# Kernel optimization log

Measured on AMD Instinct MI355X. Metric: run time of the kernel, lower is better.

Reference implementation:

```python
import jax, jax.numpy as jnp
import numpy as np

N_NODES = 100000
N_EDGES = 1600000
D_IN = 256
D_OUT = 128


def setup_inputs() -> dict:
    key = jax.random.key(0)
    ks = jax.random.split(key, 7)
    h = jax.random.normal(ks[0], (N_NODES, D_IN), dtype=jnp.float32)
    src = jax.random.randint(ks[1], (N_EDGES,), 0, N_NODES, dtype=jnp.int32)
    dst = jax.random.randint(ks[2], (N_EDGES,), 0, N_NODES, dtype=jnp.int32)
    W = jax.random.normal(ks[3], (D_IN, D_OUT), dtype=jnp.float32) * (1.0 / np.sqrt(D_IN))
    b = jax.random.normal(ks[4], (D_OUT,), dtype=jnp.float32) * 0.01
    w_att = jax.random.normal(ks[5], (2 * D_OUT, 1), dtype=jnp.float32) * (1.0 / np.sqrt(2 * D_OUT))
    b_att = jax.random.normal(ks[6], (1,), dtype=jnp.float32) * 0.01
    return {"h": h, "src": src, "dst": dst, "W": W, "b": b, "w_att": w_att, "b_att": b_att}


def reference(h, src, dst, W, b, w_att, b_att):
    # node projection: graph.ndata['h'] = self.linear(h)
    hp = h @ W + b  # [N, D_OUT]
    n = hp.shape[0]
    d = hp.shape[1]
    # edge attention: leaky_relu(att_linear(cat[h_src, h_dst]))
    # cat([hs, hd]) @ w_att == hs @ w_att[:d] + hd @ w_att[d:]  (avoids [E, 2d] concat)
    wa_s = w_att[:d, 0]  # [D_OUT]
    wa_d = w_att[d:, 0]  # [D_OUT]
    e = hp[src] @ wa_s + hp[dst] @ wa_d + b_att[0]  # [E]
    e = jax.nn.leaky_relu(e)  # default negative_slope 0.01 matches F.leaky_relu
    # segment softmax over each destination node's incoming edges
    emax = jax.ops.segment_max(e, dst, num_segments=n)  # [N]
    ex = jnp.exp(e - emax[dst])  # [E]
    denom = jax.ops.segment_sum(ex, dst, num_segments=n)  # [N]
    # weighted scatter-sum of src features: sum_e alpha_e * h_src_e
    num = jax.ops.segment_sum(ex[:, None] * hp[src], dst, num_segments=n)  # [N, D_OUT]
    out = num / jnp.where(denom > 0, denom, 1.0)[:, None]  # zero-in-degree nodes -> 0
    return out
```

## Files before the change

kernel.cpp:

```cpp
#include <hip/hip_runtime.h>
#include <hip/hip_bf16.h>

#define D_IN 256
#define D_OUT 128
#define BM 128
#define BNODES 64
#define BCAP 1536
#define EPB 8192
#define MAXNB 1600

typedef __attribute__((ext_vector_type(8))) short bf16x8;
typedef __attribute__((ext_vector_type(4))) float f32x4;

__device__ __forceinline__ unsigned short f2bf(float f) {
    unsigned u = __float_as_uint(f);
    unsigned r = ((u >> 16) & 1u) + 0x7FFFu;
    return (unsigned short)((u + r) >> 16);
}
__device__ __forceinline__ unsigned pk2(float a, float b) {
    return (unsigned)f2bf(a) | ((unsigned)f2bf(b) << 16);
}

__global__ __launch_bounds__(256) void init_bcursor_kernel(int* __restrict__ bcursor, int nb)
{
    int i = blockIdx.x * 256 + threadIdx.x;
    if (i < nb) bcursor[i] = i * BCAP;
}

__global__ __launch_bounds__(256) void prep_kernel(
    const float* __restrict__ W, unsigned short* __restrict__ WbT)
{
    int idx = blockIdx.x * 256 + threadIdx.x;
    int k = idx >> 7;
    int c = idx & 127;
    WbT[(size_t)c * 256 + k] = f2bf(W[idx]);
}

__global__ __launch_bounds__(256) void gemm_mfma_kernel(
    const float* __restrict__ h, const unsigned short* __restrict__ WbT,
    const float* __restrict__ b, const float* __restrict__ w_att,
    unsigned short* __restrict__ hpb,
    float* __restrict__ alpha_s, float* __restrict__ alpha_d, int n)
{
    __shared__ char lds[32768];
    __shared__ float als[2][BM], ald[2][BM];
    char* aT = lds;
    char* bT = lds + 16384;

    const int t    = threadIdx.x;
    const int row0 = blockIdx.x * BM;
    const int wv = t >> 6, lane = t & 63;
    const int wr = wv >> 1, wc = wv & 1;
    const int fr = lane & 15, fq = lane >> 4;

    f32x4 acc[4][4];
    #pragma unroll
    for (int m = 0; m < 4; ++m)
        #pragma unroll
        for (int nn = 0; nn < 4; ++nn) acc[m][nn] = (f32x4){0.f, 0.f, 0.f, 0.f};

    const int sr = t >> 1;
    const int sk = (t & 1) * 32;
    const size_t arow = (size_t)((row0 + sr < n) ? (row0 + sr) : (n - 1));
    const float*          asrc = h   + arow * D_IN + sk;
    const unsigned short* bsrc = WbT + (size_t)sr * D_IN + sk;
    const int   wbase = sr * 128 + sk * 2;
    const int   swz   = (sr & 7) << 4;

    for (int kb = 0; kb < 4; ++kb) {
        const float4* as = (const float4*)(asrc + kb * 64);
        #pragma unroll
        for (int c = 0; c < 4; ++c) {
            float4 v0 = as[2 * c], v1 = as[2 * c + 1];
            uint4 p;
            p.x = pk2(v0.x, v0.y); p.y = pk2(v0.z, v0.w);
            p.z = pk2(v1.x, v1.y); p.w = pk2(v1.z, v1.w);
            *(uint4*)(aT + ((wbase + c * 16) ^ swz)) = p;
        }
        const uint4* bs = (const uint4*)(bsrc + kb * 64);
        #pragma unroll
        for (int c = 0; c < 4; ++c)
            *(uint4*)(bT + ((wbase + c * 16) ^ swz)) = bs[c];
        __syncthreads();

        #pragma unroll
        for (int ks = 0; ks < 2; ++ks) {
            bf16x8 af[4], bfr[4];
            #pragma unroll
            for (int m = 0; m < 4; ++m) {
                int row = wr * 64 + m * 16 + fr;
                int o = row * 128 + ks * 64 + fq * 16;
                af[m] = *(const bf16x8*)(aT + (o ^ ((row & 7) << 4)));
            }
            #pragma unroll
            for (int nn = 0; nn < 4; ++nn) {
                int col = wc * 64 + nn * 16 + fr;
                int o = col * 128 + ks * 64 + fq * 16;
                bfr[nn] = *(const bf16x8*)(bT + (o ^ ((col & 7) << 4)));
            }
            #pragma unroll
            for (int m = 0; m < 4; ++m)
                #pragma unroll
                for (int nn = 0; nn < 4; ++nn)
                    acc[m][nn] = __builtin_amdgcn_mfma_f32_16x16x32_bf16(
                        af[m], bfr[nn], acc[m][nn], 0, 0, 0);
        }
        __syncthreads();
    }

    float bcol[4], was[4], wad[4];
    #pragma unroll
    for (int nn = 0; nn < 4; ++nn) {
        int j = wc * 64 + nn * 16 + fr;
        bcol[nn] = b[j];
        was[nn]  = w_att[j];
        wad[nn]  = w_att[D_OUT + j];
    }
    #pragma unroll
    for (int m = 0; m < 4; ++m) {
        #pragma unroll
        for (int reg = 0; reg < 4; ++reg) {
            const int lrow = wr * 64 + m * 16 + fq * 4 + reg;
            const int grow = row0 + lrow;
            float ps = 0.f, pd = 0.f;
            #pragma unroll
            for (int nn = 0; nn < 4; ++nn) {
                float vv = acc[m][nn][reg] + bcol[nn];
                ps += vv * was[nn];
                pd += vv * wad[nn];
                if (grow < n)
                    hpb[(size_t)grow * D_OUT + wc * 64 + nn * 16 + fr] = f2bf(vv);
            }
            #pragma unroll
            for (int o = 1; o < 16; o <<= 1) {
                ps += __shfl_xor(ps, o);
                pd += __shfl_xor(pd, o);
            }
            if (fr == 0) { als[wc][lrow] = ps; ald[wc][lrow] = pd; }
        }
    }
    __syncthreads();
    if (t < BM) {
        int grow = row0 + t;
        if (grow < n) {
            alpha_s[grow] = als[0][t] + als[1][t];
            alpha_d[grow] = ald[0][t] + ald[1][t];
        }
    }
}

__global__ __launch_bounds__(1024) void bucket_scatter_kernel(
    const int* __restrict__ src, const int* __restrict__ dst,
    const float* __restrict__ alpha_s, const float* __restrict__ alpha_d,
    const float* __restrict__ b_att, int* __restrict__ bcursor,
    int2* __restrict__ ebuf, int ne, int nb)
{
    __shared__ int lhist[MAXNB];
    __shared__ int gbase[MAXNB];
    __shared__ int lcur[MAXNB];
    const int t = threadIdx.x;
    for (int i = t; i < nb; i += 1024) { lhist[i] = 0; lcur[i] = 0; }
    __syncthreads();
    const int base = blockIdx.x * EPB;
    #pragma unroll
    for (int j = 0; j < EPB / 1024; ++j) {
        int idx = base + j * 1024 + t;
        if (idx < ne) atomicAdd(&lhist[dst[idx] >> 6], 1);
    }
    __syncthreads();
    for (int i = t; i < nb; i += 1024) {
        int c = lhist[i];
        gbase[i] = c ? atomicAdd(&bcursor[i], c) : 0;
    }
    __syncthreads();
    const float ba = b_att[0];
    #pragma unroll
    for (int j = 0; j < EPB / 1024; ++j) {
        int idx = base + j * 1024 + t;
        if (idx < ne) {
            int s = src[idx], d = dst[idx];
            float ev = alpha_s[s] + alpha_d[d] + ba;
            ev = (ev >= 0.f) ? ev : 0.01f * ev;
            int bkt = d >> 6;
            int pos = gbase[bkt] + atomicAdd(&lcur[bkt], 1);
            if (pos < (bkt + 1) * BCAP)
                ebuf[pos] = make_int2(s | ((d & 63) << 17), __float_as_int(ev));
        }
    }
}

#define ACCUM8(uvar, wvar)                                     \
    acc[0] += (wvar) * __uint_as_float((uvar).x << 16);        \
    acc[1] += (wvar) * __uint_as_float((uvar).x & 0xFFFF0000u);\
    acc[2] += (wvar) * __uint_as_float((uvar).y << 16);        \
    acc[3] += (wvar) * __uint_as_float((uvar).y & 0xFFFF0000u);\
    acc[4] += (wvar) * __uint_as_float((uvar).z << 16);        \
    acc[5] += (wvar) * __uint_as_float((uvar).z & 0xFFFF0000u);\
    acc[6] += (wvar) * __uint_as_float((uvar).w << 16);        \
    acc[7] += (wvar) * __uint_as_float((uvar).w & 0xFFFF0000u);

__global__ __launch_bounds__(512) void aggregate_kernel(
    const unsigned short* __restrict__ hpb, const int2* __restrict__ ebuf,
    const int* __restrict__ bcursor, float* __restrict__ out, int n)
{
    __shared__ int2 srec[BCAP];
    __shared__ int lhist[BNODES], lstart[BNODES], lcur[BNODES];
    const int t = threadIdx.x;
    const int bk = blockIdx.x;
    const int node0 = bk << 6;
    const int base = bk * BCAP;
    int cnt = bcursor[bk] - base;
    cnt = min(cnt, BCAP);

    if (t < BNODES) lhist[t] = 0;
    __syncthreads();
    for (int i = t; i < cnt; i += 512)
        atomicAdd(&lhist[(ebuf[base + i].x >> 17) & 63], 1);
    __syncthreads();
    if (t < BNODES) {
        int c0 = lhist[t];
        int incl = c0;
        #pragma unroll
        for (int o = 1; o < 64; o <<= 1) {
            int v = __shfl_up(incl, o);
            if (t >= o) incl += v;
        }
        lstart[t] = incl - c0;
        lcur[t]   = incl - c0;
    }
    __syncthreads();
    for (int i = t; i < cnt; i += 512) {
        int2 r = ebuf[base + i];
        int pos = atomicAdd(&lcur[(r.x >> 17) & 63], 1);
        srec[pos] = r;
    }
    __syncthreads();

    const int wv = t >> 6, lane = t & 63;
    const int q = lane >> 4, dlane = lane & 15;
    const uint4* hp4 = (const uint4*)hpb;

    #pragma unroll
    for (int k = 0; k < 8; ++k) {
        const int nd = wv * 8 + k;
        const int gnode = node0 + nd;
        const int off = lstart[nd], c = lhist[nd];
        float acc[8] = {0.f,0.f,0.f,0.f,0.f,0.f,0.f,0.f};
        float denom = 0.f;

        if (c > 0 && c <= 64) {
            int2 r = srec[off + min(lane, c - 1)];
            float ev = (lane < c) ? __int_as_float(r.y) : -INFINITY;
            int   sv = r.x & 0x1FFFF;
            float m = ev;
            #pragma unroll
            for (int o = 32; o; o >>= 1) m = fmaxf(m, __shfl_xor(m, o));
            float w = __expf(ev - m);
            denom = w;
            #pragma unroll
            for (int o = 32; o; o >>= 1) denom += __shfl_xor(denom, o);
            #pragma unroll 2
            for (int t0 = 0; t0 < c; t0 += 4) {
                int tt = t0 + q;
                float wq = __shfl(w, tt);
                int   sq = __shfl(sv, tt);
                uint4 u = hp4[(size_t)sq * 16 + dlane];
                ACCUM8(u, wq)
            }
            #pragma unroll
            for (int k2 = 0; k2 < 8; ++k2) {
                acc[k2] += __shfl_xor(acc[k2], 16);
                acc[k2] += __shfl_xor(acc[k2], 32);
            }
        } else if (c > 64) {
            float m = -INFINITY;
            for (int i = lane; i < c; i += 64)
                m = fmaxf(m, __int_as_float(srec[off + i].y));
            #pragma unroll
            for (int o = 32; o; o >>= 1) m = fmaxf(m, __shfl_xor(m, o));
            for (int t0 = 0; t0 < c; t0 += 4) {
                int tt = t0 + q;
                float wq = 0.f; int sq = 0;
                if (tt < c) {
                    int2 r = srec[off + tt];
                    sq = r.x & 0x1FFFF;
                    wq = __expf(__int_as_float(r.y) - m);
                }
                uint4 u = hp4[(size_t)sq * 16 + dlane];
                ACCUM8(u, wq)
                denom += wq;
            }
            #pragma unroll
            for (int k2 = 0; k2 < 8; ++k2) {
                acc[k2] += __shfl_xor(acc[k2], 16);
                acc[k2] += __shfl_xor(acc[k2], 32);
            }
            denom += __shfl_xor(denom, 16);
            denom += __shfl_xor(denom, 32);
        }

        if (q == 0 && gnode < n) {
            float inv = (c > 0) ? 1.f / denom : 0.f;
            float4 o0 = { acc[0]*inv, acc[1]*inv, acc[2]*inv, acc[3]*inv };
            float4 o1 = { acc[4]*inv, acc[5]*inv, acc[6]*inv, acc[7]*inv };
            float4* op = (float4*)(out + (size_t)gnode * D_OUT) + 2 * dlane;
            op[0] = o0;
            op[1] = o1;
        }
    }
}

extern "C" void kernel_launch(void* const* d_in, const int* in_sizes, int n_in,
                              void* d_out, int out_size, void* d_ws, size_t ws_size,
                              hipStream_t stream)
{
    const float* h     = (const float*)d_in[0];
    const int*   src   = (const int*)  d_in[1];
    const int*   dst   = (const int*)  d_in[2];
    const float* W     = (const float*)d_in[3];
    const float* b     = (const float*)d_in[4];
    const float* w_att = (const float*)d_in[5];
    const float* b_att = (const float*)d_in[6];
    float* out = (float*)d_out;

    const int n  = in_sizes[0] / D_IN;
    const int ne = in_sizes[1];
    const int nb = (n + BNODES - 1) / BNODES;

    unsigned short* hpb = (unsigned short*)d_ws;
    float* alpha_s = (float*)d_ws + (size_t)n * 64;
    float* alpha_d = alpha_s + n;
    int2*  ebuf    = (int2*)(alpha_d + n);
    int*   bcursor = (int*)(ebuf + (size_t)nb * BCAP);
    unsigned short* WbT = (unsigned short*)(bcursor + nb);

    init_bcursor_kernel<<<(nb + 255) / 256, 256, 0, stream>>>(bcursor, nb);
    prep_kernel<<<128, 256, 0, stream>>>(W, WbT);
    gemm_mfma_kernel<<<(n + BM - 1) / BM, 256, 0, stream>>>(
        h, WbT, b, w_att, hpb, alpha_s, alpha_d, n);
    bucket_scatter_kernel<<<(ne + EPB - 1) / EPB, 1024, 0, stream>>>(
        src, dst, alpha_s, alpha_d, b_att, bcursor, ebuf, ne, nb);
    aggregate_kernel<<<nb, 512, 0, stream>>>(hpb, ebuf, bcursor, out, n);
}
```

Baseline: 157.1 us.

## Prefetch GEMM tiles into registers and assign one node per quarter-wave in aggregation

The projection GEMM now loads the next K-slice of A and B into registers before running the MFMA step on the current slice, so global load latency overlaps with compute. The aggregation kernel changes from one wavefront per node, with edges split across quarter-waves and a cross-quarter reduction, to one 16-lane group per node. Each group loops over all of its node's edges serially, computing the max and the exponentials itself. This removes the shuffle reductions and the branching between the small-degree and large-degree paths. In exchange, each group walks its edges one at a time, so per-node latency grows and groups whose nodes have different degrees become imbalanced.

```diff
diff --git a/kernel.cpp b/kernel.cpp
--- a/kernel.cpp
+++ b/kernel.cpp
@@ -67,21 +67,39 @@
     const int   wbase = sr * 128 + sk * 2;
     const int   swz   = (sr & 7) << 4;
 
+    float4 a_reg[8];
+    uint4  b_reg[4];
+    {
+        const float4* ap = (const float4*)asrc;
+        #pragma unroll
+        for (int c = 0; c < 8; ++c) a_reg[c] = ap[c];
+        const uint4* bp = (const uint4*)bsrc;
+        #pragma unroll
+        for (int c = 0; c < 4; ++c) b_reg[c] = bp[c];
+    }
+
     for (int kb = 0; kb < 4; ++kb) {
-        const float4* as = (const float4*)(asrc + kb * 64);
         #pragma unroll
         for (int c = 0; c < 4; ++c) {
-            float4 v0 = as[2 * c], v1 = as[2 * c + 1];
+            float4 v0 = a_reg[2 * c], v1 = a_reg[2 * c + 1];
             uint4 p;
             p.x = pk2(v0.x, v0.y); p.y = pk2(v0.z, v0.w);
             p.z = pk2(v1.x, v1.y); p.w = pk2(v1.z, v1.w);
             *(uint4*)(aT + ((wbase + c * 16) ^ swz)) = p;
         }
-        const uint4* bs = (const uint4*)(bsrc + kb * 64);
         #pragma unroll
         for (int c = 0; c < 4; ++c)
-            *(uint4*)(bT + ((wbase + c * 16) ^ swz)) = bs[c];
+            *(uint4*)(bT + ((wbase + c * 16) ^ swz)) = b_reg[c];
         __syncthreads();
+
+        if (kb < 3) {
+            const float4* ap = (const float4*)(asrc + (kb + 1) * 64);
+            #pragma unroll
+            for (int c = 0; c < 8; ++c) a_reg[c] = ap[c];
+            const uint4* bp = (const uint4*)(bsrc + (kb + 1) * 64);
+            #pragma unroll
+            for (int c = 0; c < 4; ++c) b_reg[c] = bp[c];
+        }
 
         #pragma unroll
         for (int ks = 0; ks < 2; ++ks) {
@@ -241,65 +259,31 @@
     const uint4* hp4 = (const uint4*)hpb;
 
     #pragma unroll
-    for (int k = 0; k < 8; ++k) {
-        const int nd = wv * 8 + k;
+    for (int p = 0; p < 2; ++p) {
+        const int nd = p * 32 + wv * 4 + q;
         const int gnode = node0 + nd;
         const int off = lstart[nd], c = lhist[nd];
+
+        float m = -INFINITY;
+        for (int i = dlane; i < c; i += 16)
+            m = fmaxf(m, __int_as_float(srec[off + i].y));
+        #pragma unroll
+        for (int o = 8; o; o >>= 1) m = fmaxf(m, __shfl_xor(m, o));
+
         float acc[8] = {0.f,0.f,0.f,0.f,0.f,0.f,0.f,0.f};
         float denom = 0.f;
 
-        if (c > 0 && c <= 64) {
-            int2 r = srec[off + min(lane, c - 1)];
-            float ev = (lane < c) ? __int_as_float(r.y) : -INFINITY;
-            int   sv = r.x & 0x1FFFF;
-            float m = ev;
-            #pragma unroll
-            for (int o = 32; o; o >>= 1) m = fmaxf(m, __shfl_xor(m, o));
-            float w = __expf(ev - m);
-            denom = w;
-            #pragma unroll
-            for (int o = 32; o; o >>= 1) denom += __shfl_xor(denom, o);
-            #pragma unroll 2
-            for (int t0 = 0; t0 < c; t0 += 4) {
-                int tt = t0 + q;
-                float wq = __shfl(w, tt);
-                int   sq = __shfl(sv, tt);
-                uint4 u = hp4[(size_t)sq * 16 + dlane];
-                ACCUM8(u, wq)
-            }
-            #pragma unroll
-            for (int k2 = 0; k2 < 8; ++k2) {
-                acc[k2] += __shfl_xor(acc[k2], 16);
-                acc[k2] += __shfl_xor(acc[k2], 32);
-            }
-        } else if (c > 64) {
-            float m = -INFINITY;
-            for (int i = lane; i < c; i += 64)
-                m = fmaxf(m, __int_as_float(srec[off + i].y));
-            #pragma unroll
-            for (int o = 32; o; o >>= 1) m = fmaxf(m, __shfl_xor(m, o));
-            for (int t0 = 0; t0 < c; t0 += 4) {
-                int tt = t0 + q;
-                float wq = 0.f; int sq = 0;
-                if (tt < c) {
-                    int2 r = srec[off + tt];
-                    sq = r.x & 0x1FFFF;
-                    wq = __expf(__int_as_float(r.y) - m);
-                }
-                uint4 u = hp4[(size_t)sq * 16 + dlane];
-                ACCUM8(u, wq)
-                denom += wq;
-            }
-            #pragma unroll
-            for (int k2 = 0; k2 < 8; ++k2) {
-                acc[k2] += __shfl_xor(acc[k2], 16);
-                acc[k2] += __shfl_xor(acc[k2], 32);
-            }
-            denom += __shfl_xor(denom, 16);
-            denom += __shfl_xor(denom, 32);
-        }
-
-        if (q == 0 && gnode < n) {
+        #pragma unroll 2
+        for (int t0 = 0; t0 < c; ++t0) {
+            int2 r = srec[off + t0];
+            float w = __expf(__int_as_float(r.y) - m);
+            int s = r.x & 0x1FFFF;
+            uint4 u = hp4[(size_t)s * 16 + dlane];
+            ACCUM8(u, w)
+            denom += w;
+        }
+
+        if (gnode < n) {
             float inv = (c > 0) ? 1.f / denom : 0.f;
             float4 o0 = { acc[0]*inv, acc[1]*inv, acc[2]*inv, acc[3]*inv };
             float4 o1 = { acc[4]*inv, acc[5]*inv, acc[6]*inv, acc[7]*inv };
```

After: 164.9 us. +4.9%, slower.
